# Optimization experiments

Measured on AMD Instinct MI355X. Metric: run time of the kernel, lower is better.

The kernel has to match this reference:

```python
import jax, jax.numpy as jnp
import numpy as np

BATCH, SRC_LEN, DIM = 64, 2048, 1024


def setup_inputs() -> dict:
    key = jax.random.key(0)
    ks = jax.random.split(key, 8)
    s = 1.0 / np.sqrt(DIM)
    return {
        "source": jax.random.normal(ks[0], (BATCH, DIM), jnp.float32),
        "memory_bank": jax.random.normal(ks[1], (BATCH, SRC_LEN, DIM), jnp.float32),
        "condition": jax.random.normal(ks[2], (BATCH, DIM), jnp.float32),
        "W_query": jax.random.uniform(ks[3], (DIM, DIM), jnp.float32, -s, s),
        "b_query": jax.random.uniform(ks[4], (DIM,), jnp.float32, -s, s),
        "W_context": jax.random.uniform(ks[5], (DIM, DIM), jnp.float32, -s, s),
        "W_condition": jax.random.uniform(ks[6], (DIM, DIM), jnp.float32, -s, s),
        "v": jax.random.uniform(ks[7], (DIM,), jnp.float32, -s, s),
    }


def reference(source, memory_bank, condition, W_query, b_query, W_context, W_condition, v):
    # Bahdanau MLP score: v^T tanh(W_q q + U_a h_j + W_c cond)
    wq = source @ W_query.T + b_query                      # [b, d]
    wcond = condition @ W_condition.T                      # [b, d]
    uh = jnp.einsum('bsd,ed->bse', memory_bank, W_context) # [b, s, d]
    wquh = jnp.tanh(uh + (wq + wcond)[:, None, :])         # [b, s, d]
    align = jnp.einsum('bsd,d->bs', wquh, v)               # [b, s]
    align_vectors = jax.nn.softmax(align, axis=-1)         # [b, s]
    c = jnp.einsum('bs,bsd->bd', align_vectors, memory_bank)  # [b, d]
    return c, align_vectors[:, None, :]
```

## Files before the change

### kernel.cpp

```cpp
#include <hip/hip_runtime.h>

#define NBATCH 64
#define SRCLEN 2048
#define DIMK 1024
#define MROWS (NBATCH * SRCLEN)
#define NNB 4

typedef __attribute__((ext_vector_type(4))) float f32x4;
typedef __attribute__((ext_vector_type(8))) short bf16x8;

#define AS_GLOBAL __attribute__((address_space(1)))
#define AS_LDS __attribute__((address_space(3)))

__device__ __forceinline__ int cvt_pk_bf16(float a, float b) {
#if __has_builtin(__builtin_amdgcn_cvt_pk_bf16_f32)
  auto p = __builtin_amdgcn_cvt_pk_bf16_f32(a, b);
  return __builtin_bit_cast(int, p);
#else
  unsigned ua = __float_as_uint(a), ub = __float_as_uint(b);
  ua = (ua + 0x7fffu + ((ua >> 16) & 1u)) >> 16;
  ub = (ub + 0x7fffu + ((ub >> 16) & 1u)) & 0xffff0000u;
  return (int)(ua | ub);
#endif
}

__device__ __forceinline__ float fast_tanh(float x) {
#if __has_builtin(__builtin_amdgcn_exp2f) && __has_builtin(__builtin_amdgcn_rcpf)
  float e = __builtin_amdgcn_exp2f(x * 2.885390081777927f);
  return 1.0f - 2.0f * __builtin_amdgcn_rcpf(e + 1.0f);
#else
  float cx = fminf(15.f, fmaxf(-15.f, x));
  float e = __expf(2.0f * cx);
  return (e - 1.0f) / (e + 1.0f);
#endif
}

__global__ __launch_bounds__(256) void cvt_wc_kernel(const float* __restrict__ W,
                                                     unsigned short* __restrict__ Wb) {
  int i = (blockIdx.x * 256 + threadIdx.x) * 4;
  f32x4 x = *(const f32x4*)(W + i);
  int2 o;
  o.x = cvt_pk_bf16(x[0], x[1]);
  o.y = cvt_pk_bf16(x[2], x[3]);
  *(int2*)(Wb + i) = o;
}

__global__ __launch_bounds__(256) void bias_kernel(
    const float* __restrict__ src, const float* __restrict__ cond,
    const float* __restrict__ Wq, const float* __restrict__ bq,
    const float* __restrict__ Wcd, float* __restrict__ biasOut) {
  const int b = blockIdx.y, nb = blockIdx.x, tid = threadIdx.x;
  const int w = tid >> 6, lane = tid & 63;
  __shared__ float sl[1024], cl[1024];
  *(f32x4*)(sl + (tid << 2)) = *(const f32x4*)(src + (b << 10) + (tid << 2));
  *(f32x4*)(cl + (tid << 2)) = *(const f32x4*)(cond + (b << 10) + (tid << 2));
  __syncthreads();
  f32x4 s4[4], c4[4];
#pragma unroll
  for (int u = 0; u < 4; ++u) {
    s4[u] = *(const f32x4*)(sl + (lane << 4) + (u << 2));
    c4[u] = *(const f32x4*)(cl + (lane << 4) + (u << 2));
  }
  for (int it = 0; it < 32; ++it) {
    const int n = (nb << 7) + (w << 5) + it;
    const float* wq = Wq + (size_t)n * DIMK + (lane << 4);
    const float* wc = Wcd + (size_t)n * DIMK + (lane << 4);
    float a = 0.f;
#pragma unroll
    for (int u = 0; u < 4; ++u) {
      f32x4 q4 = *(const f32x4*)(wq + (u << 2));
      f32x4 w4 = *(const f32x4*)(wc + (u << 2));
      a += q4[0] * s4[u][0] + q4[1] * s4[u][1] + q4[2] * s4[u][2] + q4[3] * s4[u][3];
      a += w4[0] * c4[u][0] + w4[1] * c4[u][1] + w4[2] * c4[u][2] + w4[3] * c4[u][3];
    }
#pragma unroll
    for (int xm = 1; xm < 64; xm <<= 1) a += __shfl_xor(a, xm, 64);
    if (lane == 0) biasOut[(b << 10) + n] = a + bq[n];
  }
}

__global__ __launch_bounds__(256, 2) void gemm_align_kernel(
    const float* __restrict__ mb, const unsigned short* __restrict__ Wc,
    const float* __restrict__ bias, const float* __restrict__ v,
    float* __restrict__ alignP) {
  __shared__ float As[128 * 64];
  __shared__ unsigned short Bs[256 * 64];
  __shared__ float red[2][128];

  const int tid = threadIdx.x;
  const int lane = tid & 63;
  const int w = tid >> 6;
  const int wm = w & 1, wn = w >> 1;
  const int lr = lane & 15, quad = lane >> 4;
  const int nb = blockIdx.x;
  const int m0 = blockIdx.y << 7;
  const int n0 = nb << 8;

  f32x4 acc[4][8] = {};

  for (int kt = 0; kt < 16; ++kt) {
#pragma unroll
    for (int r = 0; r < 8; ++r) {
      int q = (w << 3) + r;
      int row = (q << 2) + (lane >> 4);
      int c = (lane & 15) ^ (row & 15);
      const float* g = mb + (size_t)(m0 + row) * DIMK + (kt << 6) + (c << 2);
      __builtin_amdgcn_global_load_lds((const AS_GLOBAL unsigned*)g,
                                       (AS_LDS unsigned*)(As + q * 256), 16, 0, 0);
    }
#pragma unroll
    for (int r = 0; r < 8; ++r) {
      int q = (w << 3) + r;
      int row = (q << 3) + (lane >> 3);
      int c = (lane & 7) ^ (lane >> 3);
      const unsigned short* g = Wc + (size_t)(n0 + row) * DIMK + (kt << 6) + (c << 3);
      __builtin_amdgcn_global_load_lds((const AS_GLOBAL unsigned*)g,
                                       (AS_LDS unsigned*)(Bs + q * 512), 16, 0, 0);
    }
    __syncthreads();

#pragma unroll
    for (int ks = 0; ks < 2; ++ks) {
      bf16x8 af[4];
#pragma unroll
      for (int i = 0; i < 4; ++i) {
        int row = (wm << 6) + (i << 4) + lr;
        int p0 = ((ks << 3) + (quad << 1)) ^ lr;
        f32x4 lo = *(const f32x4*)(As + (row << 6) + (p0 << 2));
        f32x4 hi = *(const f32x4*)(As + (row << 6) + ((p0 ^ 1) << 2));
        union { int i4[4]; bf16x8 v8; } u;
        u.i4[0] = cvt_pk_bf16(lo[0], lo[1]);
        u.i4[1] = cvt_pk_bf16(lo[2], lo[3]);
        u.i4[2] = cvt_pk_bf16(hi[0], hi[1]);
        u.i4[3] = cvt_pk_bf16(hi[2], hi[3]);
        af[i] = u.v8;
      }
#pragma unroll
      for (int j = 0; j < 8; ++j) {
        int row = (wn << 7) + (j << 4) + lr;
        int pb = ((ks << 2) + quad) ^ (lr & 7);
        bf16x8 bf = *(const bf16x8*)(Bs + (row << 6) + (pb << 3));
#pragma unroll
        for (int i = 0; i < 4; ++i)
          acc[i][j] = __builtin_amdgcn_mfma_f32_16x16x32_bf16(af[i], bf, acc[i][j], 0, 0, 0);
      }
    }
    __syncthreads();
  }

  const int b = m0 >> 11;
  float rowsum[4][4] = {};
#pragma unroll
  for (int j = 0; j < 8; ++j) {
    int n = n0 + (wn << 7) + (j << 4) + lr;
    float bn = bias[(b << 10) + n];
    float vn = v[n];
#pragma unroll
    for (int i = 0; i < 4; ++i)
#pragma unroll
      for (int rg = 0; rg < 4; ++rg) {
        float t = fast_tanh(acc[i][j][rg] + bn);
        rowsum[i][rg] = fmaf(t, vn, rowsum[i][rg]);
      }
  }
#pragma unroll
  for (int xm = 1; xm < 16; xm <<= 1)
#pragma unroll
    for (int i = 0; i < 4; ++i)
#pragma unroll
      for (int rg = 0; rg < 4; ++rg)
        rowsum[i][rg] += __shfl_xor(rowsum[i][rg], xm, 64);
  if (lr == 0) {
#pragma unroll
    for (int i = 0; i < 4; ++i)
#pragma unroll
      for (int rg = 0; rg < 4; ++rg)
        red[wn][(wm << 6) + (i << 4) + (quad << 2) + rg] = rowsum[i][rg];
  }
  __syncthreads();
  if (tid < 128)
    alignP[(size_t)nb * MROWS + m0 + tid] = red[0][tid] + red[1][tid];
}

__global__ __launch_bounds__(256) void softmax_kernel(const float* __restrict__ alignP,
                                                      float* __restrict__ outA) {
  const int b = blockIdx.x, tid = threadIdx.x;
  float loc[8];
  float mx = -3.0e38f;
#pragma unroll
  for (int r = 0; r < 8; ++r) {
    int s = (r << 8) + tid;
    float a = 0.f;
#pragma unroll
    for (int q = 0; q < NNB; ++q) a += alignP[(size_t)q * MROWS + (b << 11) + s];
    loc[r] = a;
    mx = fmaxf(mx, a);
  }
#pragma unroll
  for (int o = 32; o > 0; o >>= 1) mx = fmaxf(mx, __shfl_xor(mx, o, 64));
  __shared__ float sred[8];
  if ((tid & 63) == 0) sred[tid >> 6] = mx;
  __syncthreads();
  mx = fmaxf(fmaxf(sred[0], sred[1]), fmaxf(sred[2], sred[3]));
  float sum = 0.f;
#pragma unroll
  for (int r = 0; r < 8; ++r) {
    loc[r] = __expf(loc[r] - mx);
    sum += loc[r];
  }
#pragma unroll
  for (int o = 32; o > 0; o >>= 1) sum += __shfl_xor(sum, o, 64);
  __syncthreads();
  if ((tid & 63) == 0) sred[4 + (tid >> 6)] = sum;
  __syncthreads();
  sum = sred[4] + sred[5] + sred[6] + sred[7];
  float inv = 1.0f / sum;
#pragma unroll
  for (int r = 0; r < 8; ++r) outA[(b << 11) + (r << 8) + tid] = loc[r] * inv;
}

__global__ __launch_bounds__(256) void ctx_partial_kernel(const float* __restrict__ mb,
                                                          const float* __restrict__ wgt,
                                                          float* __restrict__ cP) {
  const int chunk = blockIdx.x, b = blockIdx.y, tid = threadIdx.x;
  __shared__ float wl[64];
  if (tid < 64) wl[tid] = wgt[(b << 11) + (chunk << 6) + tid];
  __syncthreads();
  const float* base = mb + ((size_t)(b << 11) + (chunk << 6)) * DIMK + (tid << 2);
  f32x4 a = {0.f, 0.f, 0.f, 0.f};
#pragma unroll 4
  for (int s = 0; s < 64; ++s) {
    f32x4 m4 = *(const f32x4*)(base + (size_t)s * DIMK);
    a += m4 * wl[s];
  }
  *(f32x4*)(cP + ((size_t)((chunk << 6) + b) << 10) + (tid << 2)) = a;
}

__global__ __launch_bounds__(256) void ctx_reduce_kernel(const float* __restrict__ cP,
                                                         float* __restrict__ out) {
  int idx = blockIdx.x * 256 + threadIdx.x;
  float s = 0.f;
#pragma unroll
  for (int c = 0; c < 32; ++c) s += cP[(size_t)(c << 16) + idx];
  out[idx] = s;
}

extern "C" void kernel_launch(void* const* d_in, const int* in_sizes, int n_in,
                              void* d_out, int out_size, void* d_ws, size_t ws_size,
                              hipStream_t stream) {
  const float* source = (const float*)d_in[0];
  const float* mb = (const float*)d_in[1];
  const float* cond = (const float*)d_in[2];
  const float* Wq = (const float*)d_in[3];
  const float* bq = (const float*)d_in[4];
  const float* Wc = (const float*)d_in[5];
  const float* Wcd = (const float*)d_in[6];
  const float* v = (const float*)d_in[7];
  float* out = (float*)d_out;

  char* ws = (char*)d_ws;
  unsigned short* Wc_bf = (unsigned short*)ws;
  float* bias = (float*)(ws + (2u << 20));
  float* alignP = (float*)(ws + (2u << 20) + (256u << 10));
  float* cP = (float*)(ws + (4u << 20) + (256u << 10));

  cvt_wc_kernel<<<1024, 256, 0, stream>>>(Wc, Wc_bf);
  bias_kernel<<<dim3(8, 64), 256, 0, stream>>>(source, cond, Wq, bq, Wcd, bias);
  gemm_align_kernel<<<dim3(NNB, 1024), 256, 0, stream>>>(mb, Wc_bf, bias, v, alignP);
  softmax_kernel<<<64, 256, 0, stream>>>(alignP, out + NBATCH * DIMK);
  ctx_partial_kernel<<<dim3(32, 64), 256, 0, stream>>>(mb, out + NBATCH * DIMK, cP);
  ctx_reduce_kernel<<<256, 256, 0, stream>>>(cP, out);
}
```

Before: 1.145 ms.

## Double-buffer GEMM LDS tiles with async prefetch and XCD-aware block swizzle

The main GEMM loop now uses two LDS buffers with K-tiles of 32. The next tile's global-to-LDS loads are issued before the current tile is computed, using explicit vmcnt waits and barriers, so memory latency overlaps with MFMA work. The grid is flattened and remapped so that consecutive blocks on the same XCD share memory_bank rows across the 4 N-blocks, which should improve L2 reuse. The swizzle patterns were reworked for the narrower tiles. The hand-written waitcnt counts are a correctness risk, and LDS use stays roughly the same.

```diff
diff --git a/kernel.cpp b/kernel.cpp
--- a/kernel.cpp
+++ b/kernel.cpp
@@ -11,6 +11,15 @@
 
 #define AS_GLOBAL __attribute__((address_space(1)))
 #define AS_LDS __attribute__((address_space(3)))
+
+#define SWAIT8() asm volatile("s_waitcnt vmcnt(8)" ::: "memory")
+#define SWAIT0() asm volatile("s_waitcnt vmcnt(0)" ::: "memory")
+#define SBAR()                              \
+  do {                                      \
+    __builtin_amdgcn_sched_barrier(0);      \
+    __builtin_amdgcn_s_barrier();           \
+    __builtin_amdgcn_sched_barrier(0);      \
+  } while (0)
 
 __device__ __forceinline__ int cvt_pk_bf16(float a, float b) {
 #if __has_builtin(__builtin_amdgcn_cvt_pk_bf16_f32)
@@ -79,12 +88,53 @@
   }
 }
 
+__device__ __forceinline__ void gemm_stage(const float* const aSrc[4],
+                                           const unsigned short* const bSrc[4], int kt,
+                                           float* Asd, unsigned short* Bsd, int w) {
+#pragma unroll
+  for (int r = 0; r < 4; ++r) {
+    int q = (w << 2) + r;
+    __builtin_amdgcn_global_load_lds((const AS_GLOBAL unsigned*)(aSrc[r] + (kt << 5)),
+                                     (AS_LDS unsigned*)(Asd + (q << 8)), 16, 0, 0);
+    __builtin_amdgcn_global_load_lds((const AS_GLOBAL unsigned*)(bSrc[r] + (kt << 5)),
+                                     (AS_LDS unsigned*)(Bsd + (q << 9)), 16, 0, 0);
+  }
+}
+
+__device__ __forceinline__ void gemm_compute(const float* Asd, const unsigned short* Bsd,
+                                             f32x4 acc[4][8], int wm, int wn, int lr,
+                                             int quad) {
+  bf16x8 af[4];
+  const int p0 = (quad << 1) ^ (lr & 7);
+  const int sc = quad ^ ((lr >> 1) & 3);
+#pragma unroll
+  for (int i = 0; i < 4; ++i) {
+    int row = (wm << 6) + (i << 4) + lr;
+    f32x4 lo = *(const f32x4*)(Asd + (row << 5) + (p0 << 2));
+    f32x4 hi = *(const f32x4*)(Asd + (row << 5) + ((p0 ^ 1) << 2));
+    union { int i4[4]; bf16x8 v8; } u;
+    u.i4[0] = cvt_pk_bf16(lo[0], lo[1]);
+    u.i4[1] = cvt_pk_bf16(lo[2], lo[3]);
+    u.i4[2] = cvt_pk_bf16(hi[0], hi[1]);
+    u.i4[3] = cvt_pk_bf16(hi[2], hi[3]);
+    af[i] = u.v8;
+  }
+#pragma unroll
+  for (int j = 0; j < 8; ++j) {
+    int row = (wn << 7) + (j << 4) + lr;
+    bf16x8 bfv = *(const bf16x8*)(Bsd + (row << 5) + (sc << 3));
+#pragma unroll
+    for (int i = 0; i < 4; ++i)
+      acc[i][j] = __builtin_amdgcn_mfma_f32_16x16x32_bf16(af[i], bfv, acc[i][j], 0, 0, 0);
+  }
+}
+
 __global__ __launch_bounds__(256, 2) void gemm_align_kernel(
     const float* __restrict__ mb, const unsigned short* __restrict__ Wc,
     const float* __restrict__ bias, const float* __restrict__ v,
     float* __restrict__ alignP) {
-  __shared__ float As[128 * 64];
-  __shared__ unsigned short Bs[256 * 64];
+  __shared__ __align__(16) float As[2][128 * 32];
+  __shared__ __align__(16) unsigned short Bs[2][256 * 32];
   __shared__ float red[2][128];
 
   const int tid = threadIdx.x;
@@ -92,63 +142,56 @@
   const int w = tid >> 6;
   const int wm = w & 1, wn = w >> 1;
   const int lr = lane & 15, quad = lane >> 4;
-  const int nb = blockIdx.x;
-  const int m0 = blockIdx.y << 7;
+
+  const int Lb = blockIdx.x;
+  const int wg = ((Lb & 7) << 9) | (Lb >> 3);
+  const int mt = wg >> 2;
+  const int nb = wg & 3;
+  const int m0 = mt << 7;
   const int n0 = nb << 8;
 
+  const float* aSrc[4];
+  const unsigned short* bSrc[4];
+#pragma unroll
+  for (int r = 0; r < 4; ++r) {
+    int q = (w << 2) + r;
+    aSrc[r] = mb + (size_t)(m0 + (q << 3) + (lane >> 3)) * DIMK +
+              (((lane & 7) ^ (lane >> 3)) << 2);
+    bSrc[r] = Wc + (size_t)(n0 + (q << 4) + (lane >> 2)) * DIMK +
+              (((lane & 3) ^ ((lane >> 3) & 3)) << 3);
+  }
+
+  float* A0 = &As[0][0];
+  float* A1 = &As[1][0];
+  unsigned short* B0 = &Bs[0][0];
+  unsigned short* B1 = &Bs[1][0];
+
   f32x4 acc[4][8] = {};
 
-  for (int kt = 0; kt < 16; ++kt) {
-#pragma unroll
-    for (int r = 0; r < 8; ++r) {
-      int q = (w << 3) + r;
-      int row = (q << 2) + (lane >> 4);
-      int c = (lane & 15) ^ (row & 15);
-      const float* g = mb + (size_t)(m0 + row) * DIMK + (kt << 6) + (c << 2);
-      __builtin_amdgcn_global_load_lds((const AS_GLOBAL unsigned*)g,
-                                       (AS_LDS unsigned*)(As + q * 256), 16, 0, 0);
-    }
-#pragma unroll
-    for (int r = 0; r < 8; ++r) {
-      int q = (w << 3) + r;
-      int row = (q << 3) + (lane >> 3);
-      int c = (lane & 7) ^ (lane >> 3);
-      const unsigned short* g = Wc + (size_t)(n0 + row) * DIMK + (kt << 6) + (c << 3);
-      __builtin_amdgcn_global_load_lds((const AS_GLOBAL unsigned*)g,
-                                       (AS_LDS unsigned*)(Bs + q * 512), 16, 0, 0);
-    }
-    __syncthreads();
-
-#pragma unroll
-    for (int ks = 0; ks < 2; ++ks) {
-      bf16x8 af[4];
-#pragma unroll
-      for (int i = 0; i < 4; ++i) {
-        int row = (wm << 6) + (i << 4) + lr;
-        int p0 = ((ks << 3) + (quad << 1)) ^ lr;
-        f32x4 lo = *(const f32x4*)(As + (row << 6) + (p0 << 2));
-        f32x4 hi = *(const f32x4*)(As + (row << 6) + ((p0 ^ 1) << 2));
-        union { int i4[4]; bf16x8 v8; } u;
-        u.i4[0] = cvt_pk_bf16(lo[0], lo[1]);
-        u.i4[1] = cvt_pk_bf16(lo[2], lo[3]);
-        u.i4[2] = cvt_pk_bf16(hi[0], hi[1]);
-        u.i4[3] = cvt_pk_bf16(hi[2], hi[3]);
-        af[i] = u.v8;
-      }
-#pragma unroll
-      for (int j = 0; j < 8; ++j) {
-        int row = (wn << 7) + (j << 4) + lr;
-        int pb = ((ks << 2) + quad) ^ (lr & 7);
-        bf16x8 bf = *(const bf16x8*)(Bs + (row << 6) + (pb << 3));
-#pragma unroll
-        for (int i = 0; i < 4; ++i)
-          acc[i][j] = __builtin_amdgcn_mfma_f32_16x16x32_bf16(af[i], bf, acc[i][j], 0, 0, 0);
-      }
-    }
-    __syncthreads();
-  }
-
-  const int b = m0 >> 11;
+  gemm_stage(aSrc, bSrc, 0, A0, B0, w);
+#pragma unroll 1
+  for (int kt = 0; kt < 30; kt += 2) {
+    gemm_stage(aSrc, bSrc, kt + 1, A1, B1, w);
+    SWAIT8();
+    SBAR();
+    gemm_compute(A0, B0, acc, wm, wn, lr, quad);
+    SBAR();
+    gemm_stage(aSrc, bSrc, kt + 2, A0, B0, w);
+    SWAIT8();
+    SBAR();
+    gemm_compute(A1, B1, acc, wm, wn, lr, quad);
+    SBAR();
+  }
+  gemm_stage(aSrc, bSrc, 31, A1, B1, w);
+  SWAIT8();
+  SBAR();
+  gemm_compute(A0, B0, acc, wm, wn, lr, quad);
+  SBAR();
+  SWAIT0();
+  SBAR();
+  gemm_compute(A1, B1, acc, wm, wn, lr, quad);
+
+  const int b = mt >> 4;
   float rowsum[4][4] = {};
 #pragma unroll
   for (int j = 0; j < 8; ++j) {
@@ -266,7 +309,7 @@
 
   cvt_wc_kernel<<<1024, 256, 0, stream>>>(Wc, Wc_bf);
   bias_kernel<<<dim3(8, 64), 256, 0, stream>>>(source, cond, Wq, bq, Wcd, bias);
-  gemm_align_kernel<<<dim3(NNB, 1024), 256, 0, stream>>>(mb, Wc_bf, bias, v, alignP);
+  gemm_align_kernel<<<4096, 256, 0, stream>>>(mb, Wc_bf, bias, v, alignP);
   softmax_kernel<<<64, 256, 0, stream>>>(alignP, out + NBATCH * DIMK);
   ctx_partial_kernel<<<dim3(32, 64), 256, 0, stream>>>(mb, out + NBATCH * DIMK, cP);
   ctx_reduce_kernel<<<256, 256, 0, stream>>>(cP, out);
```

Measured after the change: 1.224 ms. 1.07x slower.
